# Kernel tuning notes

Measured on AMD Instinct MI355X. Metric: run time of the kernel, lower is better.

The kernel has to match this reference:

```python
import jax, jax.numpy as jnp
import numpy as np

B, T, D, E, H, K = 4, 1024, 1024, 8, 4096, 2
N = B * T
EPS_LN = 1e-5
EPS_W = 1e-8
BAL_W = 0.01


def setup_inputs() -> dict:
    key = jax.random.key(0)
    ks = jax.random.split(key, 5)
    sc = 0.02
    return {
        "x": jax.random.normal(ks[0], (B, T, D), jnp.float32),
        "ln_gamma": jnp.ones((D,), jnp.float32),
        "ln_beta": jnp.zeros((D,), jnp.float32),
        "gate_w": jax.random.normal(ks[1], (D, E), jnp.float32) * sc,
        "w1": jax.random.normal(ks[2], (E, D, H), jnp.float32) * sc,
        "b1": jnp.zeros((E, H), jnp.float32),
        "w2": jax.random.normal(ks[3], (E, H, D), jnp.float32) * sc,
        "b2": jnp.zeros((E, D), jnp.float32),
    }


def reference(x, ln_gamma, ln_beta, gate_w, w1, b1, w2, b2):
    # LayerNorm (pre-norm), residual kept on raw x
    mu = jnp.mean(x, axis=-1, keepdims=True)
    var = jnp.var(x, axis=-1, keepdims=True)
    xn = (x - mu) * jax.lax.rsqrt(var + EPS_LN) * ln_gamma + ln_beta

    xf = xn.reshape(N, D)

    # Router (oscillator_state=None path): token gate only, k = top_k
    logits = xf @ gate_w                         # (N, E)
    router_probs = jax.nn.softmax(logits, axis=-1)
    top_w, top_i = jax.lax.top_k(router_probs, K)  # (N, K)
    top_w = top_w / (jnp.sum(top_w, axis=-1, keepdims=True) + EPS_W)

    # Dense per-token gate matrix: gates[n, e] = sum of top-k weights routed to e
    gates = jnp.zeros((N, E), xf.dtype).at[jnp.arange(N)[:, None], top_i].add(top_w)

    # Per-expert FFN (computed densely for all tokens, combined by sparse gates)
    h = jax.nn.gelu(jnp.einsum("nd,edh->enh", xf, w1) + b1[:, None, :], approximate=False)
    expert_out = jnp.einsum("enh,ehd->end", h, w2) + b2[:, None, :]  # (E, N, D)
    moe = jnp.einsum("ne,end->nd", gates, expert_out)

    output = x + moe.reshape(B, T, D)

    # Load-balance auxiliary loss
    counts = jnp.zeros((E,), xf.dtype).at[top_i.reshape(-1)].add(1.0)
    fraction = counts / N
    balance_loss = BAL_W * E * jnp.sum(fraction * jnp.mean(router_probs, axis=0))

    return output, balance_loss, router_probs
```

## Files before the change

kernel.cpp:

```cpp
#include <hip/hip_runtime.h>
#include <hip/hip_bf16.h>
#include <math.h>

#define DI   1024
#define EI   8
#define HI   4096
#define NI   4096

typedef __bf16 bf16x8 __attribute__((ext_vector_type(8)));
typedef float  f32x4  __attribute__((ext_vector_type(4)));

__device__ __forceinline__ unsigned short f2bf(float f) {
  union { float f; unsigned u; } c; c.f = f;
  unsigned r = c.u + 0x7FFF + ((c.u >> 16) & 1);
  return (unsigned short)(r >> 16);
}

__device__ __forceinline__ void async16(const void* g, void* l) {
  __builtin_amdgcn_global_load_lds(
      (const __attribute__((address_space(1))) void*)g,
      (__attribute__((address_space(3))) void*)l, 16, 0, 0);
}

__device__ __forceinline__ float gelu_fast(float v) {
  const float a = fabsf(v) * 0.70710678118f;
  const float t = __builtin_amdgcn_rcpf(fmaf(0.3275911f, a, 1.0f));
  float p = fmaf(1.061405429f, t, -1.453152027f);
  p = fmaf(p, t, 1.421413741f);
  p = fmaf(p, t, -0.284496736f);
  p = fmaf(p, t, 0.254829592f);
  p *= t;
  const float ex = __expf(-a * a);
  float er = fmaf(-p, ex, 1.0f);
  er = copysignf(er, v);
  return 0.5f * v * (1.0f + er);
}

#define MFMA_TILE_128(ASP, BSP)                                          \
  {                                                                      \
    _Pragma("unroll")                                                    \
    for (int kk = 0; kk < 2; kk++) {                                     \
      const int ko = ksw[kk];                                            \
      bf16x8 af[4], bfr[4];                                              \
      _Pragma("unroll")                                                  \
      for (int mi = 0; mi < 4; mi++)                                     \
        af[mi] = *(const bf16x8*)&(ASP)[(mrow + mi * 16) * 64 + ko];     \
      _Pragma("unroll")                                                  \
      for (int ni = 0; ni < 4; ni++)                                     \
        bfr[ni] = *(const bf16x8*)&(BSP)[(nrow + ni * 16) * 64 + ko];    \
      _Pragma("unroll")                                                  \
      for (int mi = 0; mi < 4; mi++)                                     \
        _Pragma("unroll")                                                \
        for (int ni = 0; ni < 4; ni++)                                   \
          acc[mi][ni] = __builtin_amdgcn_mfma_f32_16x16x32_bf16(         \
              af[mi], bfr[ni], acc[mi][ni], 0, 0, 0);                    \
    }                                                                    \
  }

__global__ __launch_bounds__(256) void ln_router_k(
    const float* __restrict__ x, const float* __restrict__ gamma,
    const float* __restrict__ beta, const float* __restrict__ gw,
    unsigned short* __restrict__ xnbf, float* __restrict__ probs_out,
    int* __restrict__ pairs, float2* __restrict__ gates2)
{
  const int t = threadIdx.x, lane = t & 63, wid = t >> 6;
  const int n = blockIdx.x * 4 + wid;

  const float4* xr = (const float4*)(x + (size_t)n * DI);
  float4 v[4];
  #pragma unroll
  for (int j = 0; j < 4; j++) v[j] = xr[lane * 4 + j];

  float s = 0.f, q = 0.f;
  #pragma unroll
  for (int j = 0; j < 4; j++) {
    s += v[j].x + v[j].y + v[j].z + v[j].w;
    q += v[j].x * v[j].x + v[j].y * v[j].y + v[j].z * v[j].z + v[j].w * v[j].w;
  }
  #pragma unroll
  for (int off = 1; off < 64; off <<= 1) {
    s += __shfl_xor(s, off);
    q += __shfl_xor(q, off);
  }
  const float mu = s * (1.0f / DI);
  const float rs = rsqrtf(q * (1.0f / DI) - mu * mu + 1e-5f);

  const float4* gr = (const float4*)gamma;
  const float4* br = (const float4*)beta;
  float xl[16];
  #pragma unroll
  for (int j = 0; j < 4; j++) {
    const float4 g4 = gr[lane * 4 + j];
    const float4 b4 = br[lane * 4 + j];
    xl[4 * j + 0] = (v[j].x - mu) * rs * g4.x + b4.x;
    xl[4 * j + 1] = (v[j].y - mu) * rs * g4.y + b4.y;
    xl[4 * j + 2] = (v[j].z - mu) * rs * g4.z + b4.z;
    xl[4 * j + 3] = (v[j].w - mu) * rs * g4.w + b4.w;
  }
  unsigned u[8];
  #pragma unroll
  for (int j = 0; j < 8; j++)
    u[j] = (unsigned)f2bf(xl[2 * j]) | ((unsigned)f2bf(xl[2 * j + 1]) << 16);
  uint4* dst = (uint4*)(xnbf + (size_t)n * DI + lane * 16);
  uint4 d0; d0.x = u[0]; d0.y = u[1]; d0.z = u[2]; d0.w = u[3];
  uint4 d1; d1.x = u[4]; d1.y = u[5]; d1.z = u[6]; d1.w = u[7];
  dst[0] = d0; dst[1] = d1;

  float p[8];
  #pragma unroll
  for (int e = 0; e < 8; e++) p[e] = 0.f;
  #pragma unroll
  for (int j = 0; j < 16; j++) {
    const float4* grow = (const float4*)(gw + (size_t)(lane * 16 + j) * EI);
    const float4 ga = grow[0], gb = grow[1];
    const float xv = xl[j];
    p[0] += xv * ga.x; p[1] += xv * ga.y; p[2] += xv * ga.z; p[3] += xv * ga.w;
    p[4] += xv * gb.x; p[5] += xv * gb.y; p[6] += xv * gb.z; p[7] += xv * gb.w;
  }
  #pragma unroll
  for (int e = 0; e < 8; e++)
    #pragma unroll
    for (int off = 1; off < 64; off <<= 1) p[e] += __shfl_xor(p[e], off);

  if (lane == 0) {
    float pm = -1e30f;
    #pragma unroll
    for (int e = 0; e < 8; e++) pm = fmaxf(pm, p[e]);
    float pr[8], ps = 0.f;
    #pragma unroll
    for (int e = 0; e < 8; e++) { pr[e] = expf(p[e] - pm); ps += pr[e]; }
    const float inv = 1.0f / ps;
    #pragma unroll
    for (int e = 0; e < 8; e++) {
      pr[e] *= inv;
      probs_out[(size_t)n * EI + e] = pr[e];
    }
    int i0 = 0; float m0 = pr[0];
    #pragma unroll
    for (int e = 1; e < 8; e++) if (pr[e] > m0) { m0 = pr[e]; i0 = e; }
    int i1 = -1; float m1 = -1e30f;
    #pragma unroll
    for (int e = 0; e < 8; e++) if (e != i0 && pr[e] > m1) { m1 = pr[e]; i1 = e; }
    const float ssum = m0 + m1 + 1e-8f;
    pairs[n] = i0 | (i1 << 8);
    float2 g2; g2.x = m0 / ssum; g2.y = m1 / ssum;
    gates2[n] = g2;
  }
}

__global__ __launch_bounds__(1024) void build_lists_k(
    const int* __restrict__ pairs, const float2* __restrict__ gates2,
    const float* __restrict__ probs, int* __restrict__ counts,
    int* __restrict__ offs, int* __restrict__ tok_list,
    float* __restrict__ gate_list, int2* __restrict__ ipos,
    float* __restrict__ out_bal)
{
  __shared__ int cnt[8];
  __shared__ int cur[8];
  __shared__ float wps[16][8];
  __shared__ float ps[8];
  const int t = threadIdx.x, lane = t & 63, wid = t >> 6;
  if (t < 8) cnt[t] = 0;
  __syncthreads();

  float acc[8];
  #pragma unroll
  for (int e = 0; e < 8; e++) acc[e] = 0.f;
  for (int n = t; n < NI; n += 1024) {
    const int pr = pairs[n];
    atomicAdd(&cnt[pr & 255], 1);
    atomicAdd(&cnt[pr >> 8], 1);
    const float4* prow = (const float4*)(probs + (size_t)n * EI);
    const float4 a = prow[0], b = prow[1];
    acc[0] += a.x; acc[1] += a.y; acc[2] += a.z; acc[3] += a.w;
    acc[4] += b.x; acc[5] += b.y; acc[6] += b.z; acc[7] += b.w;
  }
  #pragma unroll
  for (int e = 0; e < 8; e++)
    #pragma unroll
    for (int off = 1; off < 64; off <<= 1) acc[e] += __shfl_xor(acc[e], off);
  if (lane == 0)
    #pragma unroll
    for (int e = 0; e < 8; e++) wps[wid][e] = acc[e];
  __syncthreads();
  if (t < 8) {
    float sm = 0.f;
    for (int w = 0; w < 16; w++) sm += wps[w][t];
    ps[t] = sm;
  }
  __syncthreads();
  if (t == 0) {
    int off = 0; float bl = 0.f;
    for (int e = 0; e < 8; e++) {
      offs[e] = off; cur[e] = off; counts[e] = cnt[e];
      bl += (float)cnt[e] * ps[e];
      off += cnt[e];
    }
    *out_bal = 0.01f * 8.0f * bl / ((float)NI * (float)NI);
  }
  __syncthreads();
  for (int n = t; n < NI; n += 1024) {
    const int pr = pairs[n];
    const float2 g = gates2[n];
    const int p0 = atomicAdd(&cur[pr & 255], 1);
    tok_list[p0] = n; gate_list[p0] = g.x;
    const int p1 = atomicAdd(&cur[pr >> 8], 1);
    tok_list[p1] = n; gate_list[p1] = g.y;
    int2 ip; ip.x = p0; ip.y = p1;
    ipos[n] = ip;
  }
}

__global__ __launch_bounds__(256) void transpose_cvt_k(
    const float* __restrict__ in, unsigned short* __restrict__ out, int R, int C)
{
  __shared__ float tile[64][65];
  const size_t eoff = (size_t)blockIdx.z * (size_t)R * (size_t)C;
  const int c0 = blockIdx.x * 64, r0 = blockIdx.y * 64;
  const int t = threadIdx.x;
  {
    const int col = (t & 15) * 4;
    #pragma unroll
    for (int ii = 0; ii < 4; ii++) {
      const int row = (t >> 4) + ii * 16;
      const float4 v = *(const float4*)(in + eoff + (size_t)(r0 + row) * C + c0 + col);
      tile[row][col + 0] = v.x; tile[row][col + 1] = v.y;
      tile[row][col + 2] = v.z; tile[row][col + 3] = v.w;
    }
  }
  __syncthreads();
  {
    const int grp = t & 7;
    #pragma unroll
    for (int jj = 0; jj < 2; jj++) {
      const int orow = (t >> 3) + jj * 32;
      unsigned short vs[8];
      #pragma unroll
      for (int u = 0; u < 8; u++) vs[u] = f2bf(tile[grp * 8 + u][orow]);
      uint4 pk;
      pk.x = (unsigned)vs[0] | ((unsigned)vs[1] << 16);
      pk.y = (unsigned)vs[2] | ((unsigned)vs[3] << 16);
      pk.z = (unsigned)vs[4] | ((unsigned)vs[5] << 16);
      pk.w = (unsigned)vs[6] | ((unsigned)vs[7] << 16);
      *(uint4*)(out + eoff + (size_t)(c0 + orow) * R + r0 + grp * 8) = pk;
    }
  }
}

__global__ __launch_bounds__(256) void copy_x_k(const float* __restrict__ x, float* __restrict__ out)
{
  const size_t i = (size_t)blockIdx.x * 256 + threadIdx.x;
  ((float4*)out)[i] = ((const float4*)x)[i];
}

__global__ __launch_bounds__(512, 2) void ffn1_k(
    const unsigned short* __restrict__ xnbf, const unsigned short* __restrict__ w1t,
    const float* __restrict__ b1, unsigned short* __restrict__ hbuf,
    const int* __restrict__ tok_list, const int* __restrict__ counts,
    const int* __restrict__ offsets)
{
  const int e = blockIdx.z;
  const int cnt = counts[e];
  const int mt = blockIdx.y;
  if (mt * 256 >= cnt) return;
  const int n0 = blockIdx.x * 256;
  const int t = threadIdx.x, lane = t & 63, w = t >> 6;
  const int wm = w & 1, wn = w >> 1;
  __shared__ __align__(16) unsigned short As[2][256 * 64];
  __shared__ __align__(16) unsigned short Bs[2][256 * 64];

  const int sub = lane >> 3;
  const int kc  = (((lane & 7) ^ sub) * 8);
  const int eoff = offsets[e];
  const unsigned short* baseA[4];
  const unsigned short* baseB[4];
  #pragma unroll
  for (int r = 0; r < 4; r++) {
    const int row = w * 32 + r * 8 + sub;
    int idx = mt * 256 + row; if (idx > cnt - 1) idx = cnt - 1;
    const int tok = tok_list[eoff + idx];
    baseA[r] = xnbf + (size_t)tok * DI + kc;
    baseB[r] = w1t + (size_t)e * HI * DI + (size_t)(n0 + row) * DI + kc;
  }

  f32x4 acc[8][4];
  const f32x4 zz = {0.f, 0.f, 0.f, 0.f};
  #pragma unroll
  for (int i = 0; i < 8; i++)
    #pragma unroll
    for (int j = 0; j < 4; j++) acc[i][j] = zz;

  const int mrow = wm * 128 + (lane & 15);
  const int nrow = wn * 64 + (lane & 15);
  const int ksw[2] = { (((lane >> 4) ^ (lane & 7)) * 8),
                       ((((lane >> 4) + 4) ^ (lane & 7)) * 8) };

  #pragma unroll
  for (int r = 0; r < 4; r++) {
    async16(baseA[r], &As[0][(w * 32 + r * 8) * 64]);
    async16(baseB[r], &Bs[0][(w * 32 + r * 8) * 64]);
  }

  const int NT = DI / 64;
  #pragma unroll 2
  for (int ti = 0; ti < NT - 1; ++ti) {
    const int cur = ti & 1, nxt = cur ^ 1;
    __builtin_amdgcn_s_barrier();
    const int k0 = (ti + 1) * 64;
    #pragma unroll
    for (int r = 0; r < 4; r++) {
      async16(baseA[r] + k0, &As[nxt][(w * 32 + r * 8) * 64]);
      async16(baseB[r] + k0, &Bs[nxt][(w * 32 + r * 8) * 64]);
    }
    asm volatile("s_waitcnt vmcnt(8)" ::: "memory");
    __builtin_amdgcn_s_barrier();
    #pragma unroll
    for (int kk = 0; kk < 2; kk++) {
      const int ko = ksw[kk];
      bf16x8 af[8], bfr[4];
      #pragma unroll
      for (int ni = 0; ni < 4; ni++)
        bfr[ni] = *(const bf16x8*)&Bs[cur][(nrow + ni * 16) * 64 + ko];
      #pragma unroll
      for (int mi = 0; mi < 8; mi++)
        af[mi] = *(const bf16x8*)&As[cur][(mrow + mi * 16) * 64 + ko];
      #pragma unroll
      for (int mi = 0; mi < 8; mi++)
        #pragma unroll
        for (int ni = 0; ni < 4; ni++)
          acc[mi][ni] = __builtin_amdgcn_mfma_f32_16x16x32_bf16(
              af[mi], bfr[ni], acc[mi][ni], 0, 0, 0);
    }
    asm volatile("s_waitcnt lgkmcnt(0)" ::: "memory");
  }
  __builtin_amdgcn_s_barrier();
  asm volatile("s_waitcnt vmcnt(0)" ::: "memory");
  __builtin_amdgcn_s_barrier();
  {
    const int cur = (NT - 1) & 1;
    #pragma unroll
    for (int kk = 0; kk < 2; kk++) {
      const int ko = ksw[kk];
      bf16x8 af[8], bfr[4];
      #pragma unroll
      for (int ni = 0; ni < 4; ni++)
        bfr[ni] = *(const bf16x8*)&Bs[cur][(nrow + ni * 16) * 64 + ko];
      #pragma unroll
      for (int mi = 0; mi < 8; mi++)
        af[mi] = *(const bf16x8*)&As[cur][(mrow + mi * 16) * 64 + ko];
      #pragma unroll
      for (int mi = 0; mi < 8; mi++)
        #pragma unroll
        for (int ni = 0; ni < 4; ni++)
          acc[mi][ni] = __builtin_amdgcn_mfma_f32_16x16x32_bf16(
              af[mi], bfr[ni], acc[mi][ni], 0, 0, 0);
    }
  }

  const int hb = eoff + mt * 256;
  #pragma unroll
  for (int ni = 0; ni < 4; ni++) {
    const int col = n0 + wn * 64 + ni * 16 + (lane & 15);
    const float bias = b1[e * HI + col];
    #pragma unroll
    for (int mi = 0; mi < 8; mi++) {
      #pragma unroll
      for (int rg = 0; rg < 4; rg++) {
        const int rowl = wm * 128 + mi * 16 + ((lane >> 4) << 2) + rg;
        if (mt * 256 + rowl < cnt) {
          const float vv = gelu_fast(acc[mi][ni][rg] + bias);
          hbuf[(size_t)(hb + rowl) * HI + col] = f2bf(vv);
        }
      }
    }
  }
}

__global__ __launch_bounds__(256) void ffn2_k(
    const unsigned short* __restrict__ hbuf, const unsigned short* __restrict__ w2t,
    const float* __restrict__ b2, float* __restrict__ out,
    const int* __restrict__ tok_list, const float* __restrict__ gate_list,
    const int* __restrict__ counts, const int* __restrict__ offsets,
    float* __restrict__ eo)
{
  const int r  = blockIdx.x + 8 * blockIdx.y;
  const int e  = blockIdx.z;
  const int nx = r >> 5;
  const int mt = r & 31;
  const int cnt = counts[e];
  if (mt * 128 >= cnt) return;
  const int n0 = nx * 128;
  const int t = threadIdx.x, lane = t & 63, w = t >> 6;
  const int wm = w & 1, wn = w >> 1;
  __shared__ __align__(16) unsigned short As[128 * 64];
  __shared__ __align__(16) unsigned short Bs[128 * 64];

  const int sub = lane >> 3;
  const int kc = (((lane & 7) ^ sub) * 8);
  const int eoff = offsets[e];
  const int hb = eoff + mt * 128;
  const unsigned short* baseA[4];
  const unsigned short* baseB[4];
  #pragma unroll
  for (int rr = 0; rr < 4; rr++) {
    const int row = (w << 5) + rr * 8 + sub;
    baseA[rr] = hbuf + (size_t)(hb + row) * HI + kc;
    baseB[rr] = w2t + (size_t)e * DI * HI + (size_t)(n0 + row) * HI + kc;
  }

  f32x4 acc[4][4];
  const f32x4 zz = {0.f, 0.f, 0.f, 0.f};
  #pragma unroll
  for (int i = 0; i < 4; i++)
    #pragma unroll
    for (int j = 0; j < 4; j++) acc[i][j] = zz;

  const int mrow = (wm << 6) + (lane & 15);
  const int nrow = (wn << 6) + (lane & 15);
  const int ksw[2] = { (((lane >> 4) ^ (lane & 7)) * 8),
                       ((((lane >> 4) + 4) ^ (lane & 7)) * 8) };

  for (int k0 = 0; k0 < HI; k0 += 64) {
    __syncthreads();
    #pragma unroll
    for (int rr = 0; rr < 4; rr++) {
      async16(baseA[rr] + k0, &As[((w << 5) + rr * 8) * 64]);
      async16(baseB[rr] + k0, &Bs[((w << 5) + rr * 8) * 64]);
    }
    __syncthreads();
    MFMA_TILE_128(As, Bs);
  }

  float bias[4];
  #pragma unroll
  for (int ni = 0; ni < 4; ni++)
    bias[ni] = b2[e * DI + n0 + (wn << 6) + ni * 16 + (lane & 15)];

  if (eo) {
    #pragma unroll
    for (int mi = 0; mi < 4; mi++) {
      #pragma unroll
      for (int rg = 0; rg < 4; rg++) {
        const int rowl = (wm << 6) + mi * 16 + ((lane >> 4) << 2) + rg;
        const int gidx = mt * 128 + rowl;
        if (gidx < cnt) {
          float* erow = eo + (size_t)(hb + rowl) * DI;
          #pragma unroll
          for (int ni = 0; ni < 4; ni++) {
            const int col = n0 + (wn << 6) + ni * 16 + (lane & 15);
            erow[col] = acc[mi][ni][rg] + bias[ni];
          }
        }
      }
    }
  } else {
    #pragma unroll
    for (int mi = 0; mi < 4; mi++) {
      #pragma unroll
      for (int rg = 0; rg < 4; rg++) {
        const int rowl = (wm << 6) + mi * 16 + ((lane >> 4) << 2) + rg;
        const int gidx = mt * 128 + rowl;
        if (gidx < cnt) {
          const int tok = tok_list[eoff + gidx];
          const float gte = gate_list[eoff + gidx];
          float* orow = out + (size_t)tok * DI;
          #pragma unroll
          for (int ni = 0; ni < 4; ni++) {
            const int col = n0 + (wn << 6) + ni * 16 + (lane & 15);
            atomicAdd(orow + col, (acc[mi][ni][rg] + bias[ni]) * gte);
          }
        }
      }
    }
  }
}

__global__ __launch_bounds__(256) void combine_k(
    const float* __restrict__ x, const float* __restrict__ eo,
    const int2* __restrict__ ipos, const float2* __restrict__ gates2,
    float* __restrict__ out)
{
  const int n = blockIdx.x, t = threadIdx.x;
  const int2 pp = ipos[n];
  const float2 gg = gates2[n];
  const float4 a = ((const float4*)(x  + (size_t)n    * DI))[t];
  const float4 b = ((const float4*)(eo + (size_t)pp.x * DI))[t];
  const float4 c = ((const float4*)(eo + (size_t)pp.y * DI))[t];
  float4 r;
  r.x = a.x + gg.x * b.x + gg.y * c.x;
  r.y = a.y + gg.x * b.y + gg.y * c.y;
  r.z = a.z + gg.x * b.z + gg.y * c.z;
  r.w = a.w + gg.x * b.w + gg.y * c.w;
  ((float4*)(out + (size_t)n * DI))[t] = r;
}

extern "C" void kernel_launch(void* const* d_in, const int* in_sizes, int n_in,
                              void* d_out, int out_size, void* d_ws, size_t ws_size,
                              hipStream_t stream)
{
  const float* x   = (const float*)d_in[0];
  const float* gam = (const float*)d_in[1];
  const float* bet = (const float*)d_in[2];
  const float* gw  = (const float*)d_in[3];
  const float* w1  = (const float*)d_in[4];
  const float* b1  = (const float*)d_in[5];
  const float* w2  = (const float*)d_in[6];
  const float* b2  = (const float*)d_in[7];
  float* out = (float*)d_out;

  char* ws = (char*)d_ws;
  int*    counts = (int*)(ws + 0);
  int*    offs   = (int*)(ws + 64);
  int*    pairs  = (int*)(ws + 1024);
  float2* gates2 = (float2*)(ws + 20480);
  int*    tok    = (int*)(ws + 57344);
  float*  gate   = (float*)(ws + 90112);
  int2*   ipos   = (int2*)(ws + 122880);
  unsigned short* xnbf = (unsigned short*)(ws + 262656);
  unsigned short* wt   = (unsigned short*)(ws + 8651264);
  unsigned short* hbuf = (unsigned short*)(ws + 75760128);
  const bool use_eo = (ws_size >= 177472000ull);
  float* eo = use_eo ? (float*)(ws + 143917568) : (float*)nullptr;

  float* bal_out   = out + (size_t)NI * DI;
  float* probs_out = bal_out + 1;

  ln_router_k<<<NI / 4, 256, 0, stream>>>(x, gam, bet, gw, xnbf, probs_out, pairs, gates2);
  build_lists_k<<<1, 1024, 0, stream>>>(pairs, gates2, probs_out, counts, offs, tok, gate, ipos, bal_out);
  transpose_cvt_k<<<dim3(HI / 64, DI / 64, EI), 256, 0, stream>>>(w1, wt, DI, HI);
  if (!use_eo)
    copy_x_k<<<(NI * DI / 4) / 256, 256, 0, stream>>>(x, out);
  ffn1_k<<<dim3(HI / 256, 16, EI), 512, 0, stream>>>(xnbf, wt, b1, hbuf, tok, counts, offs);
  transpose_cvt_k<<<dim3(DI / 64, HI / 64, EI), 256, 0, stream>>>(w2, wt, HI, DI);
  ffn2_k<<<dim3(DI / 128, NI / 128, EI), 256, 0, stream>>>(hbuf, wt, b2, out, tok, gate, counts, offs, eo);
  if (use_eo)
    combine_k<<<NI, 256, 0, stream>>>(x, eo, ipos, gates2, out);
}
```

Baseline: 794.6 us.

## Restructure FFN GEMMs into split-K-half double-buffered pipelines with interleaved loads

Both FFN kernels now split each 64-wide K tile into two 32-wide halves in LDS with a new XOR swizzle. Global-to-LDS async loads for the next tile are interleaved between MFMA groups, using partial vmcnt waits and s_setprio around the MFMA bursts. ffn2 moves from a single-buffered 128x128 tile with 256 threads to a double-buffered 256x128 tile with 512 threads, reusing each weight tile across more tokens. The aim is to hide memory latency and cut barrier stalls, at the cost of more LDS per block, fewer ffn2 blocks, and fragile hand-tuned wait counts.

```diff
diff --git a/kernel.cpp b/kernel.cpp
--- a/kernel.cpp
+++ b/kernel.cpp
@@ -36,27 +36,6 @@
   return 0.5f * v * (1.0f + er);
 }
 
-#define MFMA_TILE_128(ASP, BSP)                                          \
-  {                                                                      \
-    _Pragma("unroll")                                                    \
-    for (int kk = 0; kk < 2; kk++) {                                     \
-      const int ko = ksw[kk];                                            \
-      bf16x8 af[4], bfr[4];                                              \
-      _Pragma("unroll")                                                  \
-      for (int mi = 0; mi < 4; mi++)                                     \
-        af[mi] = *(const bf16x8*)&(ASP)[(mrow + mi * 16) * 64 + ko];     \
-      _Pragma("unroll")                                                  \
-      for (int ni = 0; ni < 4; ni++)                                     \
-        bfr[ni] = *(const bf16x8*)&(BSP)[(nrow + ni * 16) * 64 + ko];    \
-      _Pragma("unroll")                                                  \
-      for (int mi = 0; mi < 4; mi++)                                     \
-        _Pragma("unroll")                                                \
-        for (int ni = 0; ni < 4; ni++)                                   \
-          acc[mi][ni] = __builtin_amdgcn_mfma_f32_16x16x32_bf16(         \
-              af[mi], bfr[ni], acc[mi][ni], 0, 0, 0);                    \
-    }                                                                    \
-  }
-
 __global__ __launch_bounds__(256) void ln_router_k(
     const float* __restrict__ x, const float* __restrict__ gamma,
     const float* __restrict__ beta, const float* __restrict__ gw,
@@ -266,22 +245,23 @@
   const int n0 = blockIdx.x * 256;
   const int t = threadIdx.x, lane = t & 63, w = t >> 6;
   const int wm = w & 1, wn = w >> 1;
-  __shared__ __align__(16) unsigned short As[2][256 * 64];
-  __shared__ __align__(16) unsigned short Bs[2][256 * 64];
-
-  const int sub = lane >> 3;
-  const int kc  = (((lane & 7) ^ sub) * 8);
+
+  __shared__ __align__(16) unsigned short As[2][2][8192];
+  __shared__ __align__(16) unsigned short Bs[2][2][8192];
+
   const int eoff = offsets[e];
-  const unsigned short* baseA[4];
-  const unsigned short* baseB[4];
-  #pragma unroll
-  for (int r = 0; r < 4; r++) {
-    const int row = w * 32 + r * 8 + sub;
+  const unsigned short* srcA[2];
+  const unsigned short* srcB[2];
+  #pragma unroll
+  for (int i = 0; i < 2; i++) {
+    const int row = i * 128 + (t >> 2);
+    const int col = ((t & 3) ^ ((row >> 1) & 3)) * 8;
     int idx = mt * 256 + row; if (idx > cnt - 1) idx = cnt - 1;
     const int tok = tok_list[eoff + idx];
-    baseA[r] = xnbf + (size_t)tok * DI + kc;
-    baseB[r] = w1t + (size_t)e * HI * DI + (size_t)(n0 + row) * DI + kc;
-  }
+    srcA[i] = xnbf + (size_t)tok * DI + col;
+    srcB[i] = w1t + (size_t)e * HI * DI + (size_t)(n0 + row) * DI + col;
+  }
+  const int db = (16 * w) * 32;
 
   f32x4 acc[8][4];
   const f32x4 zz = {0.f, 0.f, 0.f, 0.f};
@@ -292,70 +272,64 @@
 
   const int mrow = wm * 128 + (lane & 15);
   const int nrow = wn * 64 + (lane & 15);
-  const int ksw[2] = { (((lane >> 4) ^ (lane & 7)) * 8),
-                       ((((lane >> 4) + 4) ^ (lane & 7)) * 8) };
-
-  #pragma unroll
-  for (int r = 0; r < 4; r++) {
-    async16(baseA[r], &As[0][(w * 32 + r * 8) * 64]);
-    async16(baseB[r], &Bs[0][(w * 32 + r * 8) * 64]);
-  }
-
+  const int ko = ((lane >> 4) ^ (((lane & 15) >> 1) & 3)) * 8;
+
+  #define F1_STG_A(buf, ks, kofs) \
+    { async16(srcA[0] + (kofs) + (ks) * 32, &As[buf][ks][db]); \
+      async16(srcA[1] + (kofs) + (ks) * 32, &As[buf][ks][db + 4096]); }
+  #define F1_STG_B(buf, ks, kofs) \
+    { async16(srcB[0] + (kofs) + (ks) * 32, &Bs[buf][ks][db]); \
+      async16(srcB[1] + (kofs) + (ks) * 32, &Bs[buf][ks][db + 4096]); }
+  #define F1_LDA(buf, kk, mo) \
+    { _Pragma("unroll") for (int mi = 0; mi < 4; mi++) \
+        af[mi] = *(const bf16x8*)&As[buf][kk][(mrow + ((mo) + mi) * 16) * 32 + ko]; }
+  #define F1_LDB(buf, kk) \
+    { _Pragma("unroll") for (int ni = 0; ni < 4; ni++) \
+        bfr[ni] = *(const bf16x8*)&Bs[buf][kk][(nrow + ni * 16) * 32 + ko]; }
+  #define F1_MF(mo) \
+    { __builtin_amdgcn_s_setprio(1); \
+      _Pragma("unroll") for (int mi = 0; mi < 4; mi++) \
+        _Pragma("unroll") for (int ni = 0; ni < 4; ni++) \
+          acc[(mo) + mi][ni] = __builtin_amdgcn_mfma_f32_16x16x32_bf16( \
+              af[mi], bfr[ni], acc[(mo) + mi][ni], 0, 0, 0); \
+      __builtin_amdgcn_s_setprio(0); }
+
+  F1_STG_A(0, 0, 0) F1_STG_B(0, 0, 0) F1_STG_A(0, 1, 0) F1_STG_B(0, 1, 0)
+
+  bf16x8 af[4], bfr[4];
   const int NT = DI / 64;
-  #pragma unroll 2
   for (int ti = 0; ti < NT - 1; ++ti) {
     const int cur = ti & 1, nxt = cur ^ 1;
-    __builtin_amdgcn_s_barrier();
-    const int k0 = (ti + 1) * 64;
-    #pragma unroll
-    for (int r = 0; r < 4; r++) {
-      async16(baseA[r] + k0, &As[nxt][(w * 32 + r * 8) * 64]);
-      async16(baseB[r] + k0, &Bs[nxt][(w * 32 + r * 8) * 64]);
-    }
-    asm volatile("s_waitcnt vmcnt(8)" ::: "memory");
-    __builtin_amdgcn_s_barrier();
-    #pragma unroll
-    for (int kk = 0; kk < 2; kk++) {
-      const int ko = ksw[kk];
-      bf16x8 af[8], bfr[4];
-      #pragma unroll
-      for (int ni = 0; ni < 4; ni++)
-        bfr[ni] = *(const bf16x8*)&Bs[cur][(nrow + ni * 16) * 64 + ko];
-      #pragma unroll
-      for (int mi = 0; mi < 8; mi++)
-        af[mi] = *(const bf16x8*)&As[cur][(mrow + mi * 16) * 64 + ko];
-      #pragma unroll
-      for (int mi = 0; mi < 8; mi++)
-        #pragma unroll
-        for (int ni = 0; ni < 4; ni++)
-          acc[mi][ni] = __builtin_amdgcn_mfma_f32_16x16x32_bf16(
-              af[mi], bfr[ni], acc[mi][ni], 0, 0, 0);
-    }
-    asm volatile("s_waitcnt lgkmcnt(0)" ::: "memory");
-  }
-  __builtin_amdgcn_s_barrier();
-  asm volatile("s_waitcnt vmcnt(0)" ::: "memory");
-  __builtin_amdgcn_s_barrier();
+    const int k1 = (ti + 1) * 64;
+    F1_STG_A(nxt, 0, k1)
+    asm volatile("s_waitcnt vmcnt(6)" ::: "memory");
+    __builtin_amdgcn_s_barrier();
+    F1_LDA(cur, 0, 0) F1_LDB(cur, 0) F1_MF(0)
+    F1_STG_B(nxt, 0, k1)
+    F1_LDA(cur, 0, 4) F1_MF(4)
+    F1_STG_A(nxt, 1, k1)
+    asm volatile("s_waitcnt vmcnt(6)" ::: "memory");
+    __builtin_amdgcn_s_barrier();
+    F1_LDA(cur, 1, 0) F1_LDB(cur, 1) F1_MF(0)
+    F1_STG_B(nxt, 1, k1)
+    F1_LDA(cur, 1, 4) F1_MF(4)
+  }
   {
     const int cur = (NT - 1) & 1;
-    #pragma unroll
-    for (int kk = 0; kk < 2; kk++) {
-      const int ko = ksw[kk];
-      bf16x8 af[8], bfr[4];
-      #pragma unroll
-      for (int ni = 0; ni < 4; ni++)
-        bfr[ni] = *(const bf16x8*)&Bs[cur][(nrow + ni * 16) * 64 + ko];
-      #pragma unroll
-      for (int mi = 0; mi < 8; mi++)
-        af[mi] = *(const bf16x8*)&As[cur][(mrow + mi * 16) * 64 + ko];
-      #pragma unroll
-      for (int mi = 0; mi < 8; mi++)
-        #pragma unroll
-        for (int ni = 0; ni < 4; ni++)
-          acc[mi][ni] = __builtin_amdgcn_mfma_f32_16x16x32_bf16(
-              af[mi], bfr[ni], acc[mi][ni], 0, 0, 0);
-    }
-  }
+    asm volatile("s_waitcnt vmcnt(4)" ::: "memory");
+    __builtin_amdgcn_s_barrier();
+    F1_LDA(cur, 0, 0) F1_LDB(cur, 0) F1_MF(0)
+    F1_LDA(cur, 0, 4) F1_MF(4)
+    asm volatile("s_waitcnt vmcnt(0)" ::: "memory");
+    __builtin_amdgcn_s_barrier();
+    F1_LDA(cur, 1, 0) F1_LDB(cur, 1) F1_MF(0)
+    F1_LDA(cur, 1, 4) F1_MF(4)
+  }
+  #undef F1_STG_A
+  #undef F1_STG_B
+  #undef F1_LDA
+  #undef F1_LDB
+  #undef F1_MF
 
   const int hb = eoff + mt * 256;
   #pragma unroll
@@ -376,37 +350,40 @@
   }
 }
 
-__global__ __launch_bounds__(256) void ffn2_k(
+__global__ __launch_bounds__(512, 2) void ffn2_k(
     const unsigned short* __restrict__ hbuf, const unsigned short* __restrict__ w2t,
     const float* __restrict__ b2, float* __restrict__ out,
     const int* __restrict__ tok_list, const float* __restrict__ gate_list,
     const int* __restrict__ counts, const int* __restrict__ offsets,
     float* __restrict__ eo)
 {
-  const int r  = blockIdx.x + 8 * blockIdx.y;
-  const int e  = blockIdx.z;
-  const int nx = r >> 5;
-  const int mt = r & 31;
+  const int e = blockIdx.z;
   const int cnt = counts[e];
-  if (mt * 128 >= cnt) return;
-  const int n0 = nx * 128;
+  const int mt = blockIdx.y;
+  if (mt * 256 >= cnt) return;
+  const int n0 = blockIdx.x * 128;
   const int t = threadIdx.x, lane = t & 63, w = t >> 6;
-  const int wm = w & 1, wn = w >> 1;
-  __shared__ __align__(16) unsigned short As[128 * 64];
-  __shared__ __align__(16) unsigned short Bs[128 * 64];
-
-  const int sub = lane >> 3;
-  const int kc = (((lane & 7) ^ sub) * 8);
+  const int wm = w & 3, wn = w >> 2;
+
+  __shared__ __align__(16) unsigned short As2[2][2][8192];
+  __shared__ __align__(16) unsigned short Bs2[2][2][4096];
+
   const int eoff = offsets[e];
-  const int hb = eoff + mt * 128;
-  const unsigned short* baseA[4];
-  const unsigned short* baseB[4];
-  #pragma unroll
-  for (int rr = 0; rr < 4; rr++) {
-    const int row = (w << 5) + rr * 8 + sub;
-    baseA[rr] = hbuf + (size_t)(hb + row) * HI + kc;
-    baseB[rr] = w2t + (size_t)e * DI * HI + (size_t)(n0 + row) * HI + kc;
-  }
+  const int hb = eoff + mt * 256;
+  const unsigned short* srcA[2];
+  const unsigned short* srcB0;
+  #pragma unroll
+  for (int i = 0; i < 2; i++) {
+    const int row = i * 128 + (t >> 2);
+    const int col = ((t & 3) ^ ((row >> 1) & 3)) * 8;
+    srcA[i] = hbuf + (size_t)(hb + row) * HI + col;
+  }
+  {
+    const int row = t >> 2;
+    const int col = ((t & 3) ^ ((row >> 1) & 3)) * 8;
+    srcB0 = w2t + (size_t)e * DI * HI + (size_t)(n0 + row) * HI + col;
+  }
+  const int db = (16 * w) * 32;
 
   f32x4 acc[4][4];
   const f32x4 zz = {0.f, 0.f, 0.f, 0.f};
@@ -415,39 +392,83 @@
     #pragma unroll
     for (int j = 0; j < 4; j++) acc[i][j] = zz;
 
-  const int mrow = (wm << 6) + (lane & 15);
-  const int nrow = (wn << 6) + (lane & 15);
-  const int ksw[2] = { (((lane >> 4) ^ (lane & 7)) * 8),
-                       ((((lane >> 4) + 4) ^ (lane & 7)) * 8) };
-
-  for (int k0 = 0; k0 < HI; k0 += 64) {
-    __syncthreads();
-    #pragma unroll
-    for (int rr = 0; rr < 4; rr++) {
-      async16(baseA[rr] + k0, &As[((w << 5) + rr * 8) * 64]);
-      async16(baseB[rr] + k0, &Bs[((w << 5) + rr * 8) * 64]);
-    }
-    __syncthreads();
-    MFMA_TILE_128(As, Bs);
-  }
+  const int mrow = wm * 64 + (lane & 15);
+  const int nrow = wn * 64 + (lane & 15);
+  const int ko = ((lane >> 4) ^ (((lane & 15) >> 1) & 3)) * 8;
+
+  #define F2_STG_A(buf, ks, kofs) \
+    { async16(srcA[0] + (kofs) + (ks) * 32, &As2[buf][ks][db]); \
+      async16(srcA[1] + (kofs) + (ks) * 32, &As2[buf][ks][db + 4096]); }
+  #define F2_STG_B(buf, ks, kofs) \
+    { async16(srcB0 + (kofs) + (ks) * 32, &Bs2[buf][ks][db]); }
+  #define F2_LDA(buf, kk) \
+    { _Pragma("unroll") for (int mi = 0; mi < 4; mi++) \
+        af[mi] = *(const bf16x8*)&As2[buf][kk][(mrow + mi * 16) * 32 + ko]; }
+  #define F2_LDB(buf, kk, no) \
+    { _Pragma("unroll") for (int ni = 0; ni < 2; ni++) \
+        bfr[ni] = *(const bf16x8*)&Bs2[buf][kk][(nrow + ((no) + ni) * 16) * 32 + ko]; }
+  #define F2_MF(no) \
+    { __builtin_amdgcn_s_setprio(1); \
+      _Pragma("unroll") for (int mi = 0; mi < 4; mi++) \
+        _Pragma("unroll") for (int ni = 0; ni < 2; ni++) \
+          acc[mi][(no) + ni] = __builtin_amdgcn_mfma_f32_16x16x32_bf16( \
+              af[mi], bfr[ni], acc[mi][(no) + ni], 0, 0, 0); \
+      __builtin_amdgcn_s_setprio(0); }
+
+  F2_STG_A(0, 0, 0) F2_STG_B(0, 0, 0) F2_STG_A(0, 1, 0) F2_STG_B(0, 1, 0)
+
+  bf16x8 af[4], bfr[2];
+  const int NT = HI / 64;
+  for (int ti = 0; ti < NT - 1; ++ti) {
+    const int cur = ti & 1, nxt = cur ^ 1;
+    const int k1 = (ti + 1) * 64;
+    F2_STG_A(nxt, 0, k1)
+    asm volatile("s_waitcnt vmcnt(5)" ::: "memory");
+    __builtin_amdgcn_s_barrier();
+    F2_LDA(cur, 0) F2_LDB(cur, 0, 0) F2_MF(0)
+    F2_STG_B(nxt, 0, k1)
+    F2_LDB(cur, 0, 2) F2_MF(2)
+    F2_STG_A(nxt, 1, k1)
+    asm volatile("s_waitcnt vmcnt(5)" ::: "memory");
+    __builtin_amdgcn_s_barrier();
+    F2_LDA(cur, 1) F2_LDB(cur, 1, 0) F2_MF(0)
+    F2_STG_B(nxt, 1, k1)
+    F2_LDB(cur, 1, 2) F2_MF(2)
+  }
+  {
+    const int cur = (NT - 1) & 1;
+    asm volatile("s_waitcnt vmcnt(3)" ::: "memory");
+    __builtin_amdgcn_s_barrier();
+    F2_LDA(cur, 0) F2_LDB(cur, 0, 0) F2_MF(0)
+    F2_LDB(cur, 0, 2) F2_MF(2)
+    asm volatile("s_waitcnt vmcnt(0)" ::: "memory");
+    __builtin_amdgcn_s_barrier();
+    F2_LDA(cur, 1) F2_LDB(cur, 1, 0) F2_MF(0)
+    F2_LDB(cur, 1, 2) F2_MF(2)
+  }
+  #undef F2_STG_A
+  #undef F2_STG_B
+  #undef F2_LDA
+  #undef F2_LDB
+  #undef F2_MF
 
   float bias[4];
   #pragma unroll
   for (int ni = 0; ni < 4; ni++)
-    bias[ni] = b2[e * DI + n0 + (wn << 6) + ni * 16 + (lane & 15)];
+    bias[ni] = b2[e * DI + n0 + wn * 64 + ni * 16 + (lane & 15)];
 
   if (eo) {
     #pragma unroll
     for (int mi = 0; mi < 4; mi++) {
       #pragma unroll
       for (int rg = 0; rg < 4; rg++) {
-        const int rowl = (wm << 6) + mi * 16 + ((lane >> 4) << 2) + rg;
-        const int gidx = mt * 128 + rowl;
+        const int rowl = wm * 64 + mi * 16 + ((lane >> 4) << 2) + rg;
+        const int gidx = mt * 256 + rowl;
         if (gidx < cnt) {
           float* erow = eo + (size_t)(hb + rowl) * DI;
           #pragma unroll
           for (int ni = 0; ni < 4; ni++) {
-            const int col = n0 + (wn << 6) + ni * 16 + (lane & 15);
+            const int col = n0 + wn * 64 + ni * 16 + (lane & 15);
             erow[col] = acc[mi][ni][rg] + bias[ni];
           }
         }
@@ -458,15 +479,15 @@
     for (int mi = 0; mi < 4; mi++) {
       #pragma unroll
       for (int rg = 0; rg < 4; rg++) {
-        const int rowl = (wm << 6) + mi * 16 + ((lane >> 4) << 2) + rg;
-        const int gidx = mt * 128 + rowl;
+        const int rowl = wm * 64 + mi * 16 + ((lane >> 4) << 2) + rg;
+        const int gidx = mt * 256 + rowl;
         if (gidx < cnt) {
           const int tok = tok_list[eoff + gidx];
           const float gte = gate_list[eoff + gidx];
           float* orow = out + (size_t)tok * DI;
           #pragma unroll
           for (int ni = 0; ni < 4; ni++) {
-            const int col = n0 + (wn << 6) + ni * 16 + (lane & 15);
+            const int col = n0 + wn * 64 + ni * 16 + (lane & 15);
             atomicAdd(orow + col, (acc[mi][ni][rg] + bias[ni]) * gte);
           }
         }
@@ -532,7 +553,7 @@
     copy_x_k<<<(NI * DI / 4) / 256, 256, 0, stream>>>(x, out);
   ffn1_k<<<dim3(HI / 256, 16, EI), 512, 0, stream>>>(xnbf, wt, b1, hbuf, tok, counts, offs);
   transpose_cvt_k<<<dim3(DI / 64, HI / 64, EI), 256, 0, stream>>>(w2, wt, HI, DI);
-  ffn2_k<<<dim3(DI / 128, NI / 128, EI), 256, 0, stream>>>(hbuf, wt, b2, out, tok, gate, counts, offs, eo);
+  ffn2_k<<<dim3(DI / 128, 16, EI), 512, 0, stream>>>(hbuf, wt, b2, out, tok, gate, counts, offs, eo);
   if (use_eo)
     combine_k<<<NI, 256, 0, stream>>>(x, eo, ipos, gates2, out);
 }
```

Result: faster. 692.0 us (-12.9%).

## Double-buffer ffn2 with 256x128 tiles and 512 threads, add MFMA setprio

Applied to the files above, without the earlier changes.

ffn2 moves from a single-buffered 128x128 tile with two __syncthreads per k-step to a double-buffered 256x128 tile on 512 threads. The next k-slice is loaded asynchronously while the current one is computed, and rows past the expert's token count are clamped. Both FFN kernels now raise wave priority around their MFMA blocks with s_setprio. ffn1's pipeline is restructured to issue the next stage before compute and wait with vmcnt(0) afterward. The aim is to hide global-load latency and cut B-matrix reloads per output, at the cost of more LDS per block and possible occupancy limits.

```diff
diff --git a/kernel.cpp b/kernel.cpp
--- a/kernel.cpp
+++ b/kernel.cpp
@@ -36,27 +36,6 @@
   return 0.5f * v * (1.0f + er);
 }
 
-#define MFMA_TILE_128(ASP, BSP)                                          \
-  {                                                                      \
-    _Pragma("unroll")                                                    \
-    for (int kk = 0; kk < 2; kk++) {                                     \
-      const int ko = ksw[kk];                                            \
-      bf16x8 af[4], bfr[4];                                              \
-      _Pragma("unroll")                                                  \
-      for (int mi = 0; mi < 4; mi++)                                     \
-        af[mi] = *(const bf16x8*)&(ASP)[(mrow + mi * 16) * 64 + ko];     \
-      _Pragma("unroll")                                                  \
-      for (int ni = 0; ni < 4; ni++)                                     \
-        bfr[ni] = *(const bf16x8*)&(BSP)[(nrow + ni * 16) * 64 + ko];    \
-      _Pragma("unroll")                                                  \
-      for (int mi = 0; mi < 4; mi++)                                     \
-        _Pragma("unroll")                                                \
-        for (int ni = 0; ni < 4; ni++)                                   \
-          acc[mi][ni] = __builtin_amdgcn_mfma_f32_16x16x32_bf16(         \
-              af[mi], bfr[ni], acc[mi][ni], 0, 0, 0);                    \
-    }                                                                    \
-  }
-
 __global__ __launch_bounds__(256) void ln_router_k(
     const float* __restrict__ x, const float* __restrict__ gamma,
     const float* __restrict__ beta, const float* __restrict__ gw,
@@ -266,6 +245,7 @@
   const int n0 = blockIdx.x * 256;
   const int t = threadIdx.x, lane = t & 63, w = t >> 6;
   const int wm = w & 1, wn = w >> 1;
+
   __shared__ __align__(16) unsigned short As[2][256 * 64];
   __shared__ __align__(16) unsigned short Bs[2][256 * 64];
 
@@ -276,7 +256,7 @@
   const unsigned short* baseB[4];
   #pragma unroll
   for (int r = 0; r < 4; r++) {
-    const int row = w * 32 + r * 8 + sub;
+    const int row = (w << 5) + r * 8 + sub;
     int idx = mt * 256 + row; if (idx > cnt - 1) idx = cnt - 1;
     const int tok = tok_list[eoff + idx];
     baseA[r] = xnbf + (size_t)tok * DI + kc;
@@ -295,67 +275,51 @@
   const int ksw[2] = { (((lane >> 4) ^ (lane & 7)) * 8),
                        ((((lane >> 4) + 4) ^ (lane & 7)) * 8) };
 
-  #pragma unroll
-  for (int r = 0; r < 4; r++) {
-    async16(baseA[r], &As[0][(w * 32 + r * 8) * 64]);
-    async16(baseB[r], &Bs[0][(w * 32 + r * 8) * 64]);
-  }
-
-  const int NT = DI / 64;
-  #pragma unroll 2
-  for (int ti = 0; ti < NT - 1; ++ti) {
-    const int cur = ti & 1, nxt = cur ^ 1;
-    __builtin_amdgcn_s_barrier();
-    const int k0 = (ti + 1) * 64;
-    #pragma unroll
-    for (int r = 0; r < 4; r++) {
-      async16(baseA[r] + k0, &As[nxt][(w * 32 + r * 8) * 64]);
-      async16(baseB[r] + k0, &Bs[nxt][(w * 32 + r * 8) * 64]);
-    }
-    asm volatile("s_waitcnt vmcnt(8)" ::: "memory");
-    __builtin_amdgcn_s_barrier();
-    #pragma unroll
-    for (int kk = 0; kk < 2; kk++) {
-      const int ko = ksw[kk];
-      bf16x8 af[8], bfr[4];
-      #pragma unroll
-      for (int ni = 0; ni < 4; ni++)
-        bfr[ni] = *(const bf16x8*)&Bs[cur][(nrow + ni * 16) * 64 + ko];
-      #pragma unroll
-      for (int mi = 0; mi < 8; mi++)
-        af[mi] = *(const bf16x8*)&As[cur][(mrow + mi * 16) * 64 + ko];
-      #pragma unroll
-      for (int mi = 0; mi < 8; mi++)
-        #pragma unroll
-        for (int ni = 0; ni < 4; ni++)
-          acc[mi][ni] = __builtin_amdgcn_mfma_f32_16x16x32_bf16(
-              af[mi], bfr[ni], acc[mi][ni], 0, 0, 0);
-    }
-    asm volatile("s_waitcnt lgkmcnt(0)" ::: "memory");
-  }
-  __builtin_amdgcn_s_barrier();
+  #define F1_STAGE(buf, k0s)                                          \
+    { _Pragma("unroll")                                               \
+      for (int r = 0; r < 4; r++) {                                   \
+        async16(baseA[r] + (k0s), &As[buf][((w << 5) + r * 8) * 64]); \
+        async16(baseB[r] + (k0s), &Bs[buf][((w << 5) + r * 8) * 64]); \
+      } }
+
+  #define F1_COMPUTE(buf)                                                     \
+    { _Pragma("unroll")                                                       \
+      for (int kk = 0; kk < 2; kk++) {                                        \
+        const int ko = ksw[kk];                                               \
+        bf16x8 af[8], bfr[4];                                                 \
+        _Pragma("unroll")                                                     \
+        for (int ni = 0; ni < 4; ni++)                                        \
+          bfr[ni] = *(const bf16x8*)&Bs[buf][(nrow + ni * 16) * 64 + ko];     \
+        _Pragma("unroll")                                                     \
+        for (int mi = 0; mi < 8; mi++)                                        \
+          af[mi] = *(const bf16x8*)&As[buf][(mrow + mi * 16) * 64 + ko];      \
+        __builtin_amdgcn_s_setprio(1);                                        \
+        _Pragma("unroll")                                                     \
+        for (int mi = 0; mi < 8; mi++)                                        \
+          _Pragma("unroll")                                                   \
+          for (int ni = 0; ni < 4; ni++)                                      \
+            acc[mi][ni] = __builtin_amdgcn_mfma_f32_16x16x32_bf16(            \
+                af[mi], bfr[ni], acc[mi][ni], 0, 0, 0);                       \
+        __builtin_amdgcn_s_setprio(0);                                        \
+      } }
+
+  F1_STAGE(0, 0)
   asm volatile("s_waitcnt vmcnt(0)" ::: "memory");
   __builtin_amdgcn_s_barrier();
-  {
-    const int cur = (NT - 1) & 1;
-    #pragma unroll
-    for (int kk = 0; kk < 2; kk++) {
-      const int ko = ksw[kk];
-      bf16x8 af[8], bfr[4];
-      #pragma unroll
-      for (int ni = 0; ni < 4; ni++)
-        bfr[ni] = *(const bf16x8*)&Bs[cur][(nrow + ni * 16) * 64 + ko];
-      #pragma unroll
-      for (int mi = 0; mi < 8; mi++)
-        af[mi] = *(const bf16x8*)&As[cur][(mrow + mi * 16) * 64 + ko];
-      #pragma unroll
-      for (int mi = 0; mi < 8; mi++)
-        #pragma unroll
-        for (int ni = 0; ni < 4; ni++)
-          acc[mi][ni] = __builtin_amdgcn_mfma_f32_16x16x32_bf16(
-              af[mi], bfr[ni], acc[mi][ni], 0, 0, 0);
-    }
-  }
+
+  const int NT = DI / 64;
+  int cur = 0;
+  for (int ti = 0; ti < NT - 1; ++ti) {
+    F1_STAGE(cur ^ 1, (ti + 1) * 64)
+    F1_COMPUTE(cur)
+    asm volatile("s_waitcnt vmcnt(0)" ::: "memory");
+    __builtin_amdgcn_s_barrier();
+    cur ^= 1;
+  }
+  F1_COMPUTE(cur)
+
+  #undef F1_STAGE
+  #undef F1_COMPUTE
 
   const int hb = eoff + mt * 256;
   #pragma unroll
@@ -376,36 +340,40 @@
   }
 }
 
-__global__ __launch_bounds__(256) void ffn2_k(
+__global__ __launch_bounds__(512, 2) void ffn2_k(
     const unsigned short* __restrict__ hbuf, const unsigned short* __restrict__ w2t,
     const float* __restrict__ b2, float* __restrict__ out,
     const int* __restrict__ tok_list, const float* __restrict__ gate_list,
     const int* __restrict__ counts, const int* __restrict__ offsets,
     float* __restrict__ eo)
 {
-  const int r  = blockIdx.x + 8 * blockIdx.y;
-  const int e  = blockIdx.z;
-  const int nx = r >> 5;
-  const int mt = r & 31;
+  const int e = blockIdx.z;
   const int cnt = counts[e];
-  if (mt * 128 >= cnt) return;
-  const int n0 = nx * 128;
+  const int mt = blockIdx.y;
+  if (mt * 256 >= cnt) return;
+  const int n0 = blockIdx.x * 128;
   const int t = threadIdx.x, lane = t & 63, w = t >> 6;
-  const int wm = w & 1, wn = w >> 1;
-  __shared__ __align__(16) unsigned short As[128 * 64];
-  __shared__ __align__(16) unsigned short Bs[128 * 64];
+  const int wm = w & 3, wn = w >> 2;
+
+  __shared__ __align__(16) unsigned short As2[2][256 * 64];
+  __shared__ __align__(16) unsigned short Bs2[2][128 * 64];
 
   const int sub = lane >> 3;
   const int kc = (((lane & 7) ^ sub) * 8);
   const int eoff = offsets[e];
-  const int hb = eoff + mt * 128;
+  const int hb = eoff + mt * 256;
   const unsigned short* baseA[4];
-  const unsigned short* baseB[4];
-  #pragma unroll
-  for (int rr = 0; rr < 4; rr++) {
-    const int row = (w << 5) + rr * 8 + sub;
-    baseA[rr] = hbuf + (size_t)(hb + row) * HI + kc;
-    baseB[rr] = w2t + (size_t)e * DI * HI + (size_t)(n0 + row) * HI + kc;
+  const unsigned short* baseB[2];
+  #pragma unroll
+  for (int r = 0; r < 4; r++) {
+    const int row = (w << 5) + r * 8 + sub;
+    int idx = mt * 256 + row; if (idx > cnt - 1) idx = cnt - 1;
+    baseA[r] = hbuf + (size_t)(eoff + idx) * HI + kc;
+  }
+  #pragma unroll
+  for (int is = 0; is < 2; is++) {
+    const int row = (w << 4) + is * 8 + sub;
+    baseB[is] = w2t + (size_t)e * DI * HI + (size_t)(n0 + row) * HI + kc;
   }
 
   f32x4 acc[4][4];
@@ -415,39 +383,76 @@
     #pragma unroll
     for (int j = 0; j < 4; j++) acc[i][j] = zz;
 
-  const int mrow = (wm << 6) + (lane & 15);
-  const int nrow = (wn << 6) + (lane & 15);
+  const int mrow = wm * 64 + (lane & 15);
+  const int nrow = wn * 64 + (lane & 15);
   const int ksw[2] = { (((lane >> 4) ^ (lane & 7)) * 8),
                        ((((lane >> 4) + 4) ^ (lane & 7)) * 8) };
 
-  for (int k0 = 0; k0 < HI; k0 += 64) {
-    __syncthreads();
-    #pragma unroll
-    for (int rr = 0; rr < 4; rr++) {
-      async16(baseA[rr] + k0, &As[((w << 5) + rr * 8) * 64]);
-      async16(baseB[rr] + k0, &Bs[((w << 5) + rr * 8) * 64]);
-    }
-    __syncthreads();
-    MFMA_TILE_128(As, Bs);
-  }
+  #define F2_STAGE(buf, k0s)                                             \
+    { _Pragma("unroll")                                                  \
+      for (int r = 0; r < 4; r++)                                        \
+        async16(baseA[r] + (k0s), &As2[buf][((w << 5) + r * 8) * 64]);   \
+      _Pragma("unroll")                                                  \
+      for (int is = 0; is < 2; is++)                                     \
+        async16(baseB[is] + (k0s), &Bs2[buf][((w << 4) + is * 8) * 64]); \
+    }
+
+  #define F2_COMPUTE(buf)                                                     \
+    { _Pragma("unroll")                                                       \
+      for (int kk = 0; kk < 2; kk++) {                                        \
+        const int ko = ksw[kk];                                               \
+        bf16x8 af[4], bfr[4];                                                 \
+        _Pragma("unroll")                                                     \
+        for (int ni = 0; ni < 4; ni++)                                        \
+          bfr[ni] = *(const bf16x8*)&Bs2[buf][(nrow + ni * 16) * 64 + ko];    \
+        _Pragma("unroll")                                                     \
+        for (int mi = 0; mi < 4; mi++)                                        \
+          af[mi] = *(const bf16x8*)&As2[buf][(mrow + mi * 16) * 64 + ko];     \
+        __builtin_amdgcn_s_setprio(1);                                        \
+        _Pragma("unroll")                                                     \
+        for (int mi = 0; mi < 4; mi++)                                        \
+          _Pragma("unroll")                                                   \
+          for (int ni = 0; ni < 4; ni++)                                      \
+            acc[mi][ni] = __builtin_amdgcn_mfma_f32_16x16x32_bf16(            \
+                af[mi], bfr[ni], acc[mi][ni], 0, 0, 0);                       \
+        __builtin_amdgcn_s_setprio(0);                                        \
+      } }
+
+  F2_STAGE(0, 0)
+  asm volatile("s_waitcnt vmcnt(0)" ::: "memory");
+  __builtin_amdgcn_s_barrier();
+
+  const int NT = HI / 64;
+  int cur = 0;
+  for (int ti = 0; ti < NT - 1; ++ti) {
+    F2_STAGE(cur ^ 1, (ti + 1) * 64)
+    F2_COMPUTE(cur)
+    asm volatile("s_waitcnt vmcnt(0)" ::: "memory");
+    __builtin_amdgcn_s_barrier();
+    cur ^= 1;
+  }
+  F2_COMPUTE(cur)
+
+  #undef F2_STAGE
+  #undef F2_COMPUTE
 
   float bias[4];
   #pragma unroll
   for (int ni = 0; ni < 4; ni++)
-    bias[ni] = b2[e * DI + n0 + (wn << 6) + ni * 16 + (lane & 15)];
+    bias[ni] = b2[e * DI + n0 + wn * 64 + ni * 16 + (lane & 15)];
 
   if (eo) {
     #pragma unroll
     for (int mi = 0; mi < 4; mi++) {
       #pragma unroll
       for (int rg = 0; rg < 4; rg++) {
-        const int rowl = (wm << 6) + mi * 16 + ((lane >> 4) << 2) + rg;
-        const int gidx = mt * 128 + rowl;
+        const int rowl = wm * 64 + mi * 16 + ((lane >> 4) << 2) + rg;
+        const int gidx = mt * 256 + rowl;
         if (gidx < cnt) {
           float* erow = eo + (size_t)(hb + rowl) * DI;
           #pragma unroll
           for (int ni = 0; ni < 4; ni++) {
-            const int col = n0 + (wn << 6) + ni * 16 + (lane & 15);
+            const int col = n0 + wn * 64 + ni * 16 + (lane & 15);
             erow[col] = acc[mi][ni][rg] + bias[ni];
           }
         }
@@ -458,15 +463,15 @@
     for (int mi = 0; mi < 4; mi++) {
       #pragma unroll
       for (int rg = 0; rg < 4; rg++) {
-        const int rowl = (wm << 6) + mi * 16 + ((lane >> 4) << 2) + rg;
-        const int gidx = mt * 128 + rowl;
+        const int rowl = wm * 64 + mi * 16 + ((lane >> 4) << 2) + rg;
+        const int gidx = mt * 256 + rowl;
         if (gidx < cnt) {
           const int tok = tok_list[eoff + gidx];
           const float gte = gate_list[eoff + gidx];
           float* orow = out + (size_t)tok * DI;
           #pragma unroll
           for (int ni = 0; ni < 4; ni++) {
-            const int col = n0 + (wn << 6) + ni * 16 + (lane & 15);
+            const int col = n0 + wn * 64 + ni * 16 + (lane & 15);
             atomicAdd(orow + col, (acc[mi][ni][rg] + bias[ni]) * gte);
           }
         }
@@ -532,7 +537,7 @@
     copy_x_k<<<(NI * DI / 4) / 256, 256, 0, stream>>>(x, out);
   ffn1_k<<<dim3(HI / 256, 16, EI), 512, 0, stream>>>(xnbf, wt, b1, hbuf, tok, counts, offs);
   transpose_cvt_k<<<dim3(DI / 64, HI / 64, EI), 256, 0, stream>>>(w2, wt, HI, DI);
-  ffn2_k<<<dim3(DI / 128, NI / 128, EI), 256, 0, stream>>>(hbuf, wt, b2, out, tok, gate, counts, offs, eo);
+  ffn2_k<<<dim3(DI / 128, 16, EI), 512, 0, stream>>>(hbuf, wt, b2, out, tok, gate, counts, offs, eo);
   if (use_eo)
     combine_k<<<NI, 256, 0, stream>>>(x, eo, ipos, gates2, out);
 }
```

After: 690.2 us. 1.15x faster.
